# Optimization experiments

Hardware: AMD Instinct MI355X
Metric: run time of the kernel (lower is better)

Reference implementation:

```python
import jax, jax.numpy as jnp
import numpy as np

N, E = 50000, 800000
IN_DIM, HID, HEADS, NUM_CLASSES, NUM_GRAPHS, NUM_LAYERS = 64, 64, 4, 10000, 256, 3
OUT_W = HID * HEADS  # 256


def _gat_layer(x, src, dst, W, a_src, a_dst, b, n_nodes):
    # x: [N, in], W: [heads*out, in], a_src/a_dst: [heads, out], b: [heads*out]
    h = (x @ W.T).reshape(n_nodes, HEADS, HID)            # [N, H, D]
    s_src = jnp.einsum('nhd,hd->nh', h, a_src)            # [N, H]
    s_dst = jnp.einsum('nhd,hd->nh', h, a_dst)
    alpha = jax.nn.leaky_relu(s_src[src] + s_dst[dst], 0.2)  # [E, H]
    m = jax.ops.segment_max(alpha, dst, num_segments=n_nodes)
    m = jnp.where(jnp.isfinite(m), m, 0.0)                # isolated-node safety
    ex = jnp.exp(alpha - m[dst])
    denom = jax.ops.segment_sum(ex, dst, num_segments=n_nodes)
    w = ex / (denom[dst] + 1e-16)                         # PyG softmax epsilon
    out = jax.ops.segment_sum(h[src] * w[:, :, None], dst, num_segments=n_nodes)
    return out.reshape(n_nodes, HEADS * HID) + b


def setup_inputs() -> dict:
    key = jax.random.key(0)
    ks = jax.random.split(key, 20)
    inp = {
        'x': jax.random.normal(ks[0], (N, IN_DIM), jnp.float32),
        'edge_index': jax.random.randint(ks[1], (2, E), 0, N, jnp.int32),
        'batch': jnp.sort(jax.random.randint(ks[2], (N,), 0, NUM_GRAPHS, jnp.int32)),
        'class_label': jax.random.randint(ks[3], (NUM_GRAPHS,), 0, NUM_CLASSES, jnp.int32),
        'emb': jax.random.normal(ks[4], (NUM_CLASSES, HID), jnp.float32),
    }
    in_dims = [IN_DIM + HID, OUT_W, OUT_W]
    for l in range(NUM_LAYERS):
        kw = jax.random.split(ks[5 + l], 4)
        d_in = in_dims[l]
        sc = 1.0 / np.sqrt(d_in)
        inp[f'W{l}'] = jax.random.uniform(kw[0], (OUT_W, d_in), jnp.float32, -sc, sc)
        inp[f'asrc{l}'] = jax.random.uniform(kw[1], (HEADS, HID), jnp.float32, -sc, sc)
        inp[f'adst{l}'] = jax.random.uniform(kw[2], (HEADS, HID), jnp.float32, -sc, sc)
        inp[f'b{l}'] = jnp.zeros((OUT_W,), jnp.float32)
    sc = 1.0 / np.sqrt(OUT_W)
    inp['cls_W'] = jax.random.uniform(ks[10], (1, OUT_W), jnp.float32, -sc, sc)
    inp['cls_b'] = jnp.zeros((1,), jnp.float32)
    return inp


def reference(x, edge_index, batch, class_label, emb,
              W0, asrc0, adst0, b0,
              W1, asrc1, adst1, b1,
              W2, asrc2, adst2, b2,
              cls_W, cls_b):
    n = x.shape[0]
    # template embedding aligned per node
    t = emb[class_label][batch]                          # [N, HID]
    h = jnp.concatenate([x, t], axis=-1)                 # [N, IN+HID]
    # PyG GATConv adds self-loops by default
    loop = jnp.arange(n, dtype=edge_index.dtype)
    src = jnp.concatenate([edge_index[0], loop])
    dst = jnp.concatenate([edge_index[1], loop])
    params = [(W0, asrc0, adst0, b0), (W1, asrc1, adst1, b1), (W2, asrc2, adst2, b2)]
    for (W, a_s, a_d, b) in params:
        h = _gat_layer(h, src, dst, W, a_s, a_d, b, n)
        h = jax.nn.leaky_relu(h, 0.01)                   # F.leaky_relu default slope
    return h @ cls_W.T + cls_b                           # [N, 1]
```

## Files before the change

kernel.cpp:

```cpp
#include <hip/hip_runtime.h>
#include <hip/hip_fp16.h>
#include <math.h>

#define NNODES 50000
#define NEDGES 800000
#define NT_TILES (((NNODES + 127) / 128) * 2)
#define NGROUPS ((NNODES + 3) / 4)
#define NH0 (NNODES * 128)
#define NH04 (NH0 / 4)
#define NW4 (163840 / 4)
#define NDEG4 (NNODES / 4)
#define NPREP4 (NH04 + NW4 + NDEG4)

typedef __attribute__((ext_vector_type(8))) _Float16 f16x8;
typedef __attribute__((ext_vector_type(4))) _Float16 f16x4;
typedef __attribute__((ext_vector_type(4))) float f32x4;

static __device__ __forceinline__ void gl_lds16(const void* g, void* l) {
    __builtin_amdgcn_global_load_lds(
        (const __attribute__((address_space(1))) void*)g,
        (__attribute__((address_space(3))) void*)l, 16, 0, 0);
}

static __device__ __forceinline__ float sel4(float4 v, int head) {
    float r = v.x;
    r = (head == 1) ? v.y : r;
    r = (head == 2) ? v.z : r;
    r = (head == 3) ? v.w : r;
    return r;
}

__global__ void prep_kernel(const float* __restrict__ x,
                            const int* __restrict__ batch,
                            const int* __restrict__ class_label,
                            const float* __restrict__ emb,
                            const float* __restrict__ W0,
                            const float* __restrict__ W1,
                            const float* __restrict__ W2,
                            _Float16* __restrict__ h0,
                            _Float16* __restrict__ F0,
                            _Float16* __restrict__ F1,
                            _Float16* __restrict__ F2,
                            int* __restrict__ deg) {
    int i4 = blockIdx.x * blockDim.x + threadIdx.x;
    if (i4 < NH04) {
        int idx = i4 * 4;
        int n = idx >> 7, c = idx & 127;
        float4 v;
        if (c < 64) v = *(const float4*)&x[(n << 6) + c];
        else        v = *(const float4*)&emb[class_label[batch[n]] * 64 + (c - 64)];
        f16x4 h = {(_Float16)v.x, (_Float16)v.y, (_Float16)v.z, (_Float16)v.w};
        *(f16x4*)&h0[idx] = h;
    } else if (i4 < NH04 + NW4) {
        int i = (i4 - NH04) * 4;
        const float* src; _Float16* dst;
        if (i < 32768)       { src = W0 + i;           dst = F0 + i; }
        else if (i < 98304)  { src = W1 + (i - 32768); dst = F1 + (i - 32768); }
        else                 { src = W2 + (i - 98304); dst = F2 + (i - 98304); }
        float4 v = *(const float4*)src;
        f16x4 h = {(_Float16)v.x, (_Float16)v.y, (_Float16)v.z, (_Float16)v.w};
        *(f16x4*)dst = h;
    } else if (i4 < NPREP4) {
        int j = (i4 - NH04 - NW4) * 4;
        int4 z = {0, 0, 0, 0};
        *(int4*)&deg[j] = z;
    }
}

template <int K>
static __device__ void gemm_tile_dev(const _Float16* __restrict__ A,
                                     const _Float16* __restrict__ W,
                                     const float* __restrict__ a_src,
                                     const float* __restrict__ a_dst,
                                     _Float16* __restrict__ Cf,
                                     float* __restrict__ ssrc,
                                     float* __restrict__ sdst,
                                     char* smem, int bm, int bn) {
    const int M = NNODES;
    int tid = threadIdx.x;
    int lane = tid & 63, wave = tid >> 6;
    int wm = wave >> 1, wn = wave & 1;
    int l16 = lane & 15, quad = lane >> 4;
    int rsub = lane >> 3;
    int kcs = (lane & 7) ^ rsub;
    int sw = l16 & 7;

    f32x4 acc[4][4];
#pragma unroll
    for (int r = 0; r < 4; ++r)
#pragma unroll
        for (int c = 0; c < 4; ++c) acc[r][c] = (f32x4){0.f, 0.f, 0.f, 0.f};

    const int NST = K / 64;
    auto issue = [&](int buf, int s) {
        _Float16* dA = (_Float16*)(smem + buf * 32768);
        _Float16* dB = (_Float16*)(smem + buf * 32768 + 16384);
        int ks = s * 64;
#pragma unroll
        for (int j = 0; j < 4; ++j) {
            int seg = wave * 4 + j;
            int r = seg * 8 + rsub;
            int acol = ks + kcs * 8;
            int garow = bm + r; if (garow > M - 1) garow = M - 1;
            gl_lds16(A + (size_t)garow * K + acol, &dA[seg * 512]);
            gl_lds16(W + (size_t)(bn + r) * K + acol, &dB[seg * 512]);
        }
    };

    issue(0, 0);
    __syncthreads();
#pragma unroll
    for (int s = 0; s < NST; ++s) {
        if (s + 1 < NST) issue((s + 1) & 1, s + 1);
        const _Float16* sA = (const _Float16*)(smem + (s & 1) * 32768);
        const _Float16* sB = (const _Float16*)(smem + (s & 1) * 32768 + 16384);
#pragma unroll
        for (int ks32 = 0; ks32 < 2; ++ks32) {
            f16x8 af[4], bf[4];
#pragma unroll
            for (int r = 0; r < 4; ++r) {
                int row = wm * 64 + r * 16 + l16;
                af[r] = *(const f16x8*)&sA[row * 64 + ((ks32 * 4 + quad) ^ sw) * 8];
            }
#pragma unroll
            for (int c = 0; c < 4; ++c) {
                int row = wn * 64 + c * 16 + l16;
                bf[c] = *(const f16x8*)&sB[row * 64 + ((ks32 * 4 + quad) ^ sw) * 8];
            }
#pragma unroll
            for (int r = 0; r < 4; ++r)
#pragma unroll
                for (int c = 0; c < 4; ++c)
                    acc[r][c] = __builtin_amdgcn_mfma_f32_16x16x32_f16(
                        bf[c], af[r], acc[r][c], 0, 0, 0);
        }
        __syncthreads();
    }

    int headblk = (bn + wn * 64) >> 6;
    f32x4 av[4], dv[4];
#pragma unroll
    for (int c = 0; c < 4; ++c) {
        av[c] = *(const f32x4*)&a_src[headblk * 64 + c * 16 + quad * 4];
        dv[c] = *(const f32x4*)&a_dst[headblk * 64 + c * 16 + quad * 4];
    }
#pragma unroll
    for (int r = 0; r < 4; ++r) {
        int grow = bm + wm * 64 + r * 16 + l16;
        bool ok = grow < M;
        float ps = 0.f, pd = 0.f;
#pragma unroll
        for (int c = 0; c < 4; ++c) {
            f32x4 a = acc[r][c];
            ps += a[0] * av[c][0] + a[1] * av[c][1]
                + a[2] * av[c][2] + a[3] * av[c][3];
            pd += a[0] * dv[c][0] + a[1] * dv[c][1]
                + a[2] * dv[c][2] + a[3] * dv[c][3];
            if (ok) {
                f16x4 hv = {(_Float16)a[0], (_Float16)a[1],
                            (_Float16)a[2], (_Float16)a[3]};
                *(f16x4*)&Cf[(size_t)grow * 256 + bn + wn * 64 + c * 16 + quad * 4] = hv;
            }
        }
        ps += __shfl_xor(ps, 16, 64);
        ps += __shfl_xor(ps, 32, 64);
        pd += __shfl_xor(pd, 16, 64);
        pd += __shfl_xor(pd, 32, 64);
        if (quad == 0 && ok) {
            ssrc[grow * 4 + headblk] = ps;
            sdst[grow * 4 + headblk] = pd;
        }
    }
}

template <int K>
__global__ __launch_bounds__(256) void gemm_mfma_kernel(
        const _Float16* __restrict__ A, const _Float16* __restrict__ W,
        const float* __restrict__ a_src, const float* __restrict__ a_dst,
        _Float16* __restrict__ Cf,
        float* __restrict__ ssrc, float* __restrict__ sdst) {
    __shared__ __align__(16) char smem[65536];
    gemm_tile_dev<K>(A, W, a_src, a_dst, Cf, ssrc, sdst, smem,
                     blockIdx.x * 128, blockIdx.y * 128);
}

__global__ __launch_bounds__(256) void gemm0_bucket_kernel(
        const _Float16* __restrict__ A, const _Float16* __restrict__ W,
        const float* __restrict__ a_src, const float* __restrict__ a_dst,
        _Float16* __restrict__ Cf,
        float* __restrict__ ssrc, float* __restrict__ sdst,
        const int* __restrict__ ei,
        int* __restrict__ deg, int* __restrict__ slots) {
    __shared__ __align__(16) char smem[65536];
    int b = blockIdx.x;
    if ((b & 1) == 0) {
        int tile = b >> 1;
        if (tile < NT_TILES)
            gemm_tile_dev<128>(A, W, a_src, a_dst, Cf, ssrc, sdst, smem,
                               (tile >> 1) * 128, (tile & 1) * 128);
    } else {
        int rel = b >> 1;
        int stride = NT_TILES * 256;
        for (int e = rel * 256 + (int)threadIdx.x; e < NEDGES; e += stride) {
            int d = ei[NEDGES + e];
            int pos = atomicAdd(&deg[d], 1);
            if (pos < 64) slots[(size_t)d * 64 + pos] = ei[e];
        }
    }
}

template <bool LAST>
__global__ __launch_bounds__(256) void aggregate_kernel(
        const _Float16* __restrict__ hpf,
        const float* __restrict__ ssrc,
        const float* __restrict__ sdst,
        const int* __restrict__ deg,
        const int* __restrict__ slots,
        const float* __restrict__ bias,
        _Float16* __restrict__ out_h,
        const float* __restrict__ cls_W,
        const float* __restrict__ cls_b,
        float* __restrict__ out) {
    __shared__ __align__(16) float s_w[4][64][4];
    __shared__ int s_idx[4][64];
    int lane = threadIdx.x & 63;
    int slot = threadIdx.x >> 6;
    int n = blockIdx.x * 4 + slot;
    if (n >= NNODES) return;
    int head = lane >> 4;
    int dn = deg[n]; if (dn > 64) dn = 64;
    float4 sd = ((const float4*)sdst)[n];
    const f16x4* hp4 = (const f16x4*)hpf;

    float4 ssl = ((const float4*)ssrc)[n];
    float ax = ssl.x + sd.x, ay = ssl.y + sd.y;
    float az = ssl.z + sd.z, aw = ssl.w + sd.w;
    ax = ax > 0.f ? ax : 0.2f * ax;
    ay = ay > 0.f ? ay : 0.2f * ay;
    az = az > 0.f ? az : 0.2f * az;
    aw = aw > 0.f ? aw : 0.2f * aw;
    float4 exs = {__expf(ax), __expf(ay), __expf(az), __expf(aw)};
    float wself = sel4(exs, head);
    f16x4 vs = hp4[(size_t)n * 64 + lane];
    float dsum = wself;
    float4 acc = {wself * (float)vs.x, wself * (float)vs.y,
                  wself * (float)vs.z, wself * (float)vs.w};

    float4 ex = {0.f, 0.f, 0.f, 0.f};
    int s = 0;
    if (lane < dn) {
        s = slots[(size_t)n * 64 + lane];
        float4 ss = ((const float4*)ssrc)[s];
        float bx = ss.x + sd.x, by = ss.y + sd.y;
        float bz = ss.z + sd.z, bw = ss.w + sd.w;
        bx = bx > 0.f ? bx : 0.2f * bx;
        by = by > 0.f ? by : 0.2f * by;
        bz = bz > 0.f ? bz : 0.2f * bz;
        bw = bw > 0.f ? bw : 0.2f * bw;
        ex.x = __expf(bx); ex.y = __expf(by);
        ex.z = __expf(bz); ex.w = __expf(bw);
    }
    *(float4*)&s_w[slot][lane][0] = ex;
    s_idx[slot][lane] = s;

    int e = 0;
    for (; e + 8 <= dn; e += 8) {
        int si[8]; float w[8]; f16x4 v[8];
#pragma unroll
        for (int t = 0; t < 8; ++t) {
            si[t] = s_idx[slot][e + t];
            w[t] = s_w[slot][e + t][head];
        }
#pragma unroll
        for (int t = 0; t < 8; ++t) v[t] = hp4[(size_t)si[t] * 64 + lane];
#pragma unroll
        for (int t = 0; t < 8; ++t) {
            dsum += w[t];
            acc.x += w[t] * (float)v[t].x;
            acc.y += w[t] * (float)v[t].y;
            acc.z += w[t] * (float)v[t].z;
            acc.w += w[t] * (float)v[t].w;
        }
    }
    for (; e < dn; ++e) {
        int si = s_idx[slot][e];
        float w = s_w[slot][e][head];
        f16x4 v = hp4[(size_t)si * 64 + lane];
        dsum += w;
        acc.x += w * (float)v.x; acc.y += w * (float)v.y;
        acc.z += w * (float)v.z; acc.w += w * (float)v.w;
    }

    float inv = 1.f / (dsum + 1e-16f);
    float4 bv = ((const float4*)bias)[lane];
    float4 o;
    o.x = acc.x * inv + bv.x;
    o.y = acc.y * inv + bv.y;
    o.z = acc.z * inv + bv.z;
    o.w = acc.w * inv + bv.w;
    o.x = o.x > 0.f ? o.x : 0.01f * o.x;
    o.y = o.y > 0.f ? o.y : 0.01f * o.y;
    o.z = o.z > 0.f ? o.z : 0.01f * o.z;
    o.w = o.w > 0.f ? o.w : 0.01f * o.w;

    if (!LAST) {
        f16x4 ov = {(_Float16)o.x, (_Float16)o.y, (_Float16)o.z, (_Float16)o.w};
        ((f16x4*)out_h)[(size_t)n * 64 + lane] = ov;
    } else {
        float4 wv = ((const float4*)cls_W)[lane];
        float sdot = o.x * wv.x + o.y * wv.y + o.z * wv.z + o.w * wv.w;
#pragma unroll
        for (int off = 1; off < 64; off <<= 1)
            sdot += __shfl_xor(sdot, off, 64);
        if (lane == 0) out[n] = sdot + cls_b[0];
    }
}

extern "C" void kernel_launch(void* const* d_in, const int* in_sizes, int n_in,
                              void* d_out, int out_size, void* d_ws, size_t ws_size,
                              hipStream_t stream) {
    const float* x     = (const float*)d_in[0];
    const int*   ei    = (const int*)d_in[1];
    const int*   batch = (const int*)d_in[2];
    const int*   clab  = (const int*)d_in[3];
    const float* emb   = (const float*)d_in[4];
    const float* W[3]    = {(const float*)d_in[5], (const float*)d_in[9],  (const float*)d_in[13]};
    const float* asrc[3] = {(const float*)d_in[6], (const float*)d_in[10], (const float*)d_in[14]};
    const float* adst[3] = {(const float*)d_in[7], (const float*)d_in[11], (const float*)d_in[15]};
    const float* bias[3] = {(const float*)d_in[8], (const float*)d_in[12], (const float*)d_in[16]};
    const float* clsW = (const float*)d_in[17];
    const float* clsb = (const float*)d_in[18];
    float* out = (float*)d_out;

    char* ws = (char*)d_ws;
    size_t off = 0;
    auto alloc = [&](size_t bytes) {
        void* p = ws + off;
        off += (bytes + 255) & ~(size_t)255;
        return p;
    };
    _Float16* Cf   = (_Float16*)alloc((size_t)NNODES * 256 * 2);
    _Float16* hA   = (_Float16*)alloc((size_t)NNODES * 256 * 2);
    _Float16* h0f  = (_Float16*)alloc((size_t)NNODES * 128 * 2);
    _Float16* Wf[3];
    Wf[0] = (_Float16*)alloc((size_t)256 * 128 * 2);
    Wf[1] = (_Float16*)alloc((size_t)256 * 256 * 2);
    Wf[2] = (_Float16*)alloc((size_t)256 * 256 * 2);
    float* ssrc  = (float*)alloc((size_t)NNODES * 4 * 4);
    float* sdst  = (float*)alloc((size_t)NNODES * 4 * 4);
    int*   deg   = (int*)alloc((size_t)NNODES * 4);
    int*   slots = (int*)alloc((size_t)NNODES * 64 * 4);
    (void)ws_size; (void)in_sizes; (void)n_in; (void)out_size;

    prep_kernel<<<dim3((NPREP4 + 255) / 256), dim3(256), 0, stream>>>(
        x, batch, clab, emb, W[0], W[1], W[2], h0f, Wf[0], Wf[1], Wf[2], deg);

    dim3 gemm_grid((NNODES + 127) / 128, 2);
    dim3 node_grid(NGROUPS);

    gemm0_bucket_kernel<<<dim3(NT_TILES * 2), dim3(256), 0, stream>>>(
        h0f, Wf[0], asrc[0], adst[0], Cf, ssrc, sdst, ei, deg, slots);
    aggregate_kernel<false><<<node_grid, dim3(256), 0, stream>>>(
        Cf, ssrc, sdst, deg, slots, bias[0], hA, nullptr, nullptr, nullptr);

    gemm_mfma_kernel<256><<<gemm_grid, dim3(256), 0, stream>>>(
        hA, Wf[1], asrc[1], adst[1], Cf, ssrc, sdst);
    aggregate_kernel<false><<<node_grid, dim3(256), 0, stream>>>(
        Cf, ssrc, sdst, deg, slots, bias[1], hA, nullptr, nullptr, nullptr);

    gemm_mfma_kernel<256><<<gemm_grid, dim3(256), 0, stream>>>(
        hA, Wf[2], asrc[2], adst[2], Cf, ssrc, sdst);
    aggregate_kernel<true><<<node_grid, dim3(256), 0, stream>>>(
        Cf, ssrc, sdst, deg, slots, bias[2], nullptr, clsW, clsb, out);
}
```

Before: 373.4 us.

## Halve GEMM K-stage depth and LDS footprint to raise occupancy

The MFMA GEMM now stages 32-wide K slices instead of 64-wide ones. It uses a new row-pair swizzled LDS layout, which halves shared memory per block from 64KB to 32KB. Launch bounds ask for 4 blocks per CU so more waves can overlap the global-to-LDS loads. In exchange there are twice as many pipeline stages and barriers per tile, and the register cap may cause spills.

```diff
diff --git a/kernel.cpp b/kernel.cpp
--- a/kernel.cpp
+++ b/kernel.cpp
@@ -81,9 +81,13 @@
     int lane = tid & 63, wave = tid >> 6;
     int wm = wave >> 1, wn = wave & 1;
     int l16 = lane & 15, quad = lane >> 4;
-    int rsub = lane >> 3;
-    int kcs = (lane & 7) ^ rsub;
-    int sw = l16 & 7;
+
+    int srp_lo = lane >> 3;
+    int rbit = (lane >> 2) & 1;
+    int slot = lane & 3;
+
+    int halfrow = l16 >> 1, rb = l16 & 1, swz = halfrow & 3;
+    int qsw = quad ^ swz;
 
     f32x4 acc[4][4];
 #pragma unroll
@@ -91,19 +95,21 @@
 #pragma unroll
         for (int c = 0; c < 4; ++c) acc[r][c] = (f32x4){0.f, 0.f, 0.f, 0.f};
 
-    const int NST = K / 64;
+    const int NST = K / 32;
     auto issue = [&](int buf, int s) {
-        _Float16* dA = (_Float16*)(smem + buf * 32768);
-        _Float16* dB = (_Float16*)(smem + buf * 32768 + 16384);
-        int ks = s * 64;
-#pragma unroll
-        for (int j = 0; j < 4; ++j) {
-            int seg = wave * 4 + j;
-            int r = seg * 8 + rsub;
-            int acol = ks + kcs * 8;
-            int garow = bm + r; if (garow > M - 1) garow = M - 1;
-            gl_lds16(A + (size_t)garow * K + acol, &dA[seg * 512]);
-            gl_lds16(W + (size_t)(bn + r) * K + acol, &dB[seg * 512]);
+        _Float16* dA = (_Float16*)(smem + buf * 16384);
+        _Float16* dB = (_Float16*)(smem + buf * 16384 + 8192);
+        int ks = s * 32;
+#pragma unroll
+        for (int j = 0; j < 2; ++j) {
+            int seg = wave * 2 + j;
+            int rowpair = seg * 8 + srp_lo;
+            int row = rowpair * 2 + rbit;
+            int kc = slot ^ (rowpair & 3);
+            int col = ks + kc * 8;
+            int garow = bm + row; if (garow > M - 1) garow = M - 1;
+            gl_lds16(A + (size_t)garow * K + col, &dA[seg * 512]);
+            gl_lds16(W + (size_t)(bn + row) * K + col, &dB[seg * 512]);
         }
     };
 
@@ -112,28 +118,25 @@
 #pragma unroll
     for (int s = 0; s < NST; ++s) {
         if (s + 1 < NST) issue((s + 1) & 1, s + 1);
-        const _Float16* sA = (const _Float16*)(smem + (s & 1) * 32768);
-        const _Float16* sB = (const _Float16*)(smem + (s & 1) * 32768 + 16384);
-#pragma unroll
-        for (int ks32 = 0; ks32 < 2; ++ks32) {
-            f16x8 af[4], bf[4];
-#pragma unroll
-            for (int r = 0; r < 4; ++r) {
-                int row = wm * 64 + r * 16 + l16;
-                af[r] = *(const f16x8*)&sA[row * 64 + ((ks32 * 4 + quad) ^ sw) * 8];
-            }
-#pragma unroll
-            for (int c = 0; c < 4; ++c) {
-                int row = wn * 64 + c * 16 + l16;
-                bf[c] = *(const f16x8*)&sB[row * 64 + ((ks32 * 4 + quad) ^ sw) * 8];
-            }
-#pragma unroll
-            for (int r = 0; r < 4; ++r)
-#pragma unroll
-                for (int c = 0; c < 4; ++c)
-                    acc[r][c] = __builtin_amdgcn_mfma_f32_16x16x32_f16(
-                        bf[c], af[r], acc[r][c], 0, 0, 0);
-        }
+        const _Float16* sA = (const _Float16*)(smem + (s & 1) * 16384);
+        const _Float16* sB = (const _Float16*)(smem + (s & 1) * 16384 + 8192);
+        f16x8 af[4], bf[4];
+#pragma unroll
+        for (int r = 0; r < 4; ++r) {
+            int rowpair = wm * 32 + r * 8 + halfrow;
+            af[r] = *(const f16x8*)&sA[(rowpair * 8 + rb * 4 + qsw) * 8];
+        }
+#pragma unroll
+        for (int c = 0; c < 4; ++c) {
+            int rowpair = wn * 32 + c * 8 + halfrow;
+            bf[c] = *(const f16x8*)&sB[(rowpair * 8 + rb * 4 + qsw) * 8];
+        }
+#pragma unroll
+        for (int r = 0; r < 4; ++r)
+#pragma unroll
+            for (int c = 0; c < 4; ++c)
+                acc[r][c] = __builtin_amdgcn_mfma_f32_16x16x32_f16(
+                    bf[c], af[r], acc[r][c], 0, 0, 0);
         __syncthreads();
     }
 
@@ -174,24 +177,24 @@
 }
 
 template <int K>
-__global__ __launch_bounds__(256) void gemm_mfma_kernel(
+__global__ __launch_bounds__(256, 4) void gemm_mfma_kernel(
         const _Float16* __restrict__ A, const _Float16* __restrict__ W,
         const float* __restrict__ a_src, const float* __restrict__ a_dst,
         _Float16* __restrict__ Cf,
         float* __restrict__ ssrc, float* __restrict__ sdst) {
-    __shared__ __align__(16) char smem[65536];
+    __shared__ __align__(16) char smem[32768];
     gemm_tile_dev<K>(A, W, a_src, a_dst, Cf, ssrc, sdst, smem,
                      blockIdx.x * 128, blockIdx.y * 128);
 }
 
-__global__ __launch_bounds__(256) void gemm0_bucket_kernel(
+__global__ __launch_bounds__(256, 4) void gemm0_bucket_kernel(
         const _Float16* __restrict__ A, const _Float16* __restrict__ W,
         const float* __restrict__ a_src, const float* __restrict__ a_dst,
         _Float16* __restrict__ Cf,
         float* __restrict__ ssrc, float* __restrict__ sdst,
         const int* __restrict__ ei,
         int* __restrict__ deg, int* __restrict__ slots) {
-    __shared__ __align__(16) char smem[65536];
+    __shared__ __align__(16) char smem[32768];
     int b = blockIdx.x;
     if ((b & 1) == 0) {
         int tile = b >> 1;
```

After: 385.3 us. +3.2%, slower.
